# Performance work log

Hardware: AMD Instinct MI355X
Metric: run time of the kernel (lower is better)

## Reference

```python
import jax, jax.numpy as jnp
import numpy as np

N_NODES = 50000
N_EDGES = 800000
IN_DIM = 64
EDGE_DIM = 2
HID = 128
NUM_LAYERS = 4
NUM_GRAPHS = 128
BN_EPS = 1e-5


def setup_inputs() -> dict:
    key = jax.random.key(0)
    ks = jax.random.split(key, 24)
    s = 0.05
    inp = {
        "x": jax.random.normal(ks[0], (N_NODES, IN_DIM), jnp.float32),
        "edge_attr": jax.random.normal(ks[1], (N_EDGES, EDGE_DIM), jnp.float32),
        "edge_index": jax.random.randint(ks[2], (2, N_EDGES), 0, N_NODES, jnp.int32),
        "batch": jnp.sort(jax.random.randint(ks[3], (N_NODES,), 0, NUM_GRAPHS, jnp.int32)),
        # parameters
        "W_in": jax.random.normal(ks[4], (IN_DIM, HID), jnp.float32) * s,
        "b_in": jnp.zeros((HID,), jnp.float32),
        "W_e": jax.random.normal(ks[5], (EDGE_DIM, HID), jnp.float32) * s,
        "b_e": jnp.zeros((HID,), jnp.float32),
        "conv_W1": jax.random.normal(ks[6], (NUM_LAYERS, HID, HID), jnp.float32) * s,
        "conv_b1": jnp.zeros((NUM_LAYERS, HID), jnp.float32),
        "conv_W2": jax.random.normal(ks[7], (NUM_LAYERS, HID, HID), jnp.float32) * s,
        "conv_b2": jnp.zeros((NUM_LAYERS, HID), jnp.float32),
        "bn_g": jnp.ones((NUM_LAYERS, HID), jnp.float32),
        "bn_b": jnp.zeros((NUM_LAYERS, HID), jnp.float32),
        "vn_W1": jax.random.normal(ks[8], (HID, HID), jnp.float32) * s,
        "vn_b1": jnp.zeros((HID,), jnp.float32),
        "vn_W2": jax.random.normal(ks[9], (HID, HID), jnp.float32) * s,
        "vn_b2": jnp.zeros((HID,), jnp.float32),
        "cls_W1": jax.random.normal(ks[10], (HID, HID), jnp.float32) * s,
        "cls_b1": jnp.zeros((HID,), jnp.float32),
        "cls_W2": jax.random.normal(ks[11], (HID, 1), jnp.float32) * s,
        "cls_b2": jnp.zeros((1,), jnp.float32),
    }
    return inp


def reference(x, edge_attr, W_in, b_in, W_e, b_e, conv_W1, conv_b1, conv_W2, conv_b2,
              bn_g, bn_b, vn_W1, vn_b1, vn_W2, vn_b2, cls_W1, cls_b1, cls_W2, cls_b2,
              edge_index, batch):
    seg = jax.ops.segment_sum
    n = x.shape[0]
    src, dst = edge_index[0], edge_index[1]

    h = x @ W_in + b_in                      # [N, H]
    e = edge_attr @ W_e + b_e                # [E, H]
    vn = jnp.zeros((NUM_GRAPHS, HID), h.dtype)

    for i in range(NUM_LAYERS):
        h = h + vn[batch]                    # virtual-node broadcast
        # GINEConv (eps=0): msg = relu(x_j + e); aggregate-sum at dst; mlp(x_i + aggr)
        m = jax.nn.relu(h[src] + e)          # [E, H]
        aggr = seg(m, dst, num_segments=n)   # [N, H]
        z = h + aggr
        z = jax.nn.relu(z @ conv_W1[i] + conv_b1[i]) @ conv_W2[i] + conv_b2[i]
        # BatchNorm1d over node dim (batch statistics, biased variance)
        mu = jnp.mean(z, axis=0)
        var = jnp.mean(jnp.square(z - mu), axis=0)
        z = (z - mu) * jax.lax.rsqrt(var + BN_EPS) * bn_g[i] + bn_b[i]
        h = jax.nn.relu(z)                   # dropout disabled (deterministic)
        if i != NUM_LAYERS - 1:
            vn_up = seg(h, batch, num_segments=NUM_GRAPHS)   # global_add_pool
            vn = vn + (jax.nn.relu(vn_up @ vn_W1 + vn_b1) @ vn_W2 + vn_b2)

    # global_mean_pool
    counts = seg(jnp.ones((n,), h.dtype), batch, num_segments=NUM_GRAPHS)
    g = seg(h, batch, num_segments=NUM_GRAPHS) / jnp.maximum(counts, 1.0)[:, None]
    logits = (jax.nn.relu(g @ cls_W1 + cls_b1) @ cls_W2 + cls_b2).reshape(-1)
    return logits
```

## Files before the change

kernel.cpp:

```cpp
#include <hip/hip_runtime.h>

#define N_NODES 50000
#define N_EDGES 800000
#define IN_DIM 64
#define HID 128
#define NUM_LAYERS 4
#define NUM_GRAPHS 128
#define BN_EPS 1e-5f

typedef __attribute__((ext_vector_type(8))) short short8;
typedef __attribute__((ext_vector_type(4))) float f32x4;

__device__ inline unsigned short f2bf(float f) {
    unsigned int u = __float_as_uint(f);
    u += 0x7FFFu + ((u >> 16) & 1u);
    return (unsigned short)(u >> 16);
}
__device__ inline float bflo(unsigned int p) { return __uint_as_float(p << 16); }
__device__ inline float bfhi(unsigned int p) { return __uint_as_float(p & 0xFFFF0000u); }
__device__ inline float bfch(const uint4& v, int c) {
    unsigned int p = (&v.x)[c >> 1];
    return (c & 1) ? bfhi(p) : bflo(p);
}


__global__ void hist_kernel(const int* __restrict__ dst, int* __restrict__ cnt,
                            int* __restrict__ rank) {
    int base = blockIdx.x * 1024 + threadIdx.x;
#pragma unroll
    for (int u = 0; u < 4; ++u) {
        int e = base + u * 256;
        if (e < N_EDGES) rank[e] = atomicAdd(&cnt[dst[e]], 1);
    }
}

__global__ void endpos_kernel(const int* __restrict__ batch, int* __restrict__ endpos) {
    int n = blockIdx.x * 256 + threadIdx.x;
    if (n >= N_NODES) return;
    int b = batch[n];
    int b1 = (n + 1 < N_NODES) ? batch[n + 1] : NUM_GRAPHS;
    for (int g = b; g < b1; ++g) endpos[g] = n + 1;
    if (n == 0)
        for (int g = 0; g < b; ++g) endpos[g] = 0;
}

__global__ void wprep_kernel(const float* __restrict__ W_in,
                             const float* __restrict__ conv_W1,
                             const float* __restrict__ conv_W2,
                             unsigned short* __restrict__ wt_in,
                             unsigned short* __restrict__ wt1,
                             unsigned short* __restrict__ wt2) {
    int i = blockIdx.x * 256 + threadIdx.x;
    if (i < 128 * IN_DIM) {
        int c = i >> 6, k = i & 63;
        wt_in[i] = f2bf(W_in[k * HID + c]);
    }
    if (i < 4 * HID * HID) {
        int o = i & (HID * HID - 1);
        int layer = i >> 14;
        int c = o >> 7, k = o & 127;
        wt1[i] = f2bf(conv_W1[layer * HID * HID + k * HID + c]);
        wt2[i] = f2bf(conv_W2[layer * HID * HID + k * HID + c]);
    }
}

#define SCAN_BLOCKS ((N_NODES + 1023) / 1024)

__global__ __launch_bounds__(1024) void scan1_kernel(const int* __restrict__ cnt,
                                                     int* __restrict__ bsum) {
    __shared__ int ls[1024];
    int t = threadIdx.x;
    int g = blockIdx.x * 1024 + t;
    int v = (g < N_NODES) ? cnt[g] : 0;
    ls[t] = v;
    __syncthreads();
    for (int off = 512; off > 0; off >>= 1) {
        if (t < off) ls[t] += ls[t + off];
        __syncthreads();
    }
    if (t == 0) bsum[blockIdx.x] = ls[0];
}

__global__ void scan2_kernel(const int* __restrict__ bsum, int* __restrict__ boff) {
    if (threadIdx.x == 0) {
        int r = 0;
        for (int i = 0; i < SCAN_BLOCKS; ++i) {
            boff[i] = r;
            r += bsum[i];
        }
    }
}

__global__ __launch_bounds__(1024) void scan3_kernel(const int* __restrict__ cnt,
                                                     const int* __restrict__ boff,
                                                     int* __restrict__ row_start) {
    __shared__ int ls[1024];
    int t = threadIdx.x;
    int g = blockIdx.x * 1024 + t;
    int v = (g < N_NODES) ? cnt[g] : 0;
    ls[t] = v;
    __syncthreads();
    for (int off = 1; off < 1024; off <<= 1) {
        int x = (t >= off) ? ls[t - off] : 0;
        __syncthreads();
        ls[t] += x;
        __syncthreads();
    }
    int excl = ls[t] - v + boff[blockIdx.x];
    if (g < N_NODES) {
        row_start[g] = excl;
        if (g == N_NODES - 1) row_start[N_NODES] = excl + v;
    }
}

__global__ void fill_kernel(const int* __restrict__ src, const int* __restrict__ dst,
                            const float* __restrict__ ea, const int* __restrict__ rank,
                            const int* __restrict__ row_start, int4* __restrict__ edges) {
    int e = blockIdx.x * 256 + threadIdx.x;
    if (e >= N_EDGES) return;
    float2 a = *(const float2*)&ea[2 * e];
    int p = row_start[dst[e]] + rank[e];
    edges[p] = make_int4(src[e], __float_as_int(a.x), __float_as_int(a.y), 0);
}

__global__ void hvadd_kernel(const unsigned short* __restrict__ hbf,
                             const unsigned short* __restrict__ vnb,
                             const int* __restrict__ batch,
                             unsigned short* __restrict__ gbf) {
    int idx = blockIdx.x * 256 + threadIdx.x;
    int n = idx >> 4;
    if (n >= N_NODES) return;
    int cg = (idx & 15) * 8;
    uint4 h = *(const uint4*)&hbf[(size_t)n * HID + cg];
    uint4 v = *(const uint4*)&vnb[(size_t)batch[n] * HID + cg];
    unsigned int o[4];
#pragma unroll
    for (int p = 0; p < 4; ++p) {
        float lo = bflo((&h.x)[p]) + bflo((&v.x)[p]);
        float hi = bfhi((&h.x)[p]) + bfhi((&v.x)[p]);
        o[p] = (unsigned int)f2bf(lo) | ((unsigned int)f2bf(hi) << 16);
    }
    *(uint4*)&gbf[(size_t)n * HID + cg] = make_uint4(o[0], o[1], o[2], o[3]);
}

__global__ __launch_bounds__(256) void aggr_kernel(const unsigned short* __restrict__ gbf,
                                                   const int4* __restrict__ edges,
                                                   const int* __restrict__ row_start,
                                                   const float* __restrict__ We,
                                                   const float* __restrict__ be,
                                                   unsigned short* __restrict__ zbf,
                                                   float* __restrict__ S1,
                                                   float* __restrict__ S2) {
    int tid = threadIdx.x;
    if (blockIdx.x == 0 && tid < HID) {
        S1[tid] = 0.f;
        S2[tid] = 0.f;
    }
    int cg = (tid & 15) * 8;
    int n = blockIdx.x * 16 + (tid >> 4);

    float w0[8], w1[8], bc[8];
    {
        float4 a0 = *(const float4*)&We[cg], a1 = *(const float4*)&We[cg + 4];
        float4 b0 = *(const float4*)&We[HID + cg], b1v = *(const float4*)&We[HID + cg + 4];
        float4 c0 = *(const float4*)&be[cg], c1 = *(const float4*)&be[cg + 4];
        w0[0]=a0.x; w0[1]=a0.y; w0[2]=a0.z; w0[3]=a0.w; w0[4]=a1.x; w0[5]=a1.y; w0[6]=a1.z; w0[7]=a1.w;
        w1[0]=b0.x; w1[1]=b0.y; w1[2]=b0.z; w1[3]=b0.w; w1[4]=b1v.x; w1[5]=b1v.y; w1[6]=b1v.z; w1[7]=b1v.w;
        bc[0]=c0.x; bc[1]=c0.y; bc[2]=c0.z; bc[3]=c0.w; bc[4]=c1.x; bc[5]=c1.y; bc[6]=c1.z; bc[7]=c1.w;
    }

    uint4 hs = *(const uint4*)&gbf[(size_t)n * HID + cg];
    int jb = row_start[n], je = row_start[n + 1];
    float acc[8];
#pragma unroll
    for (int c = 0; c < 8; ++c) acc[c] = 0.f;

    int j = jb;
    for (; j + 8 <= je; j += 8) {
        int4 q[8];
        uint4 hq[8];
#pragma unroll
        for (int u = 0; u < 8; ++u) q[u] = edges[j + u];
#pragma unroll
        for (int u = 0; u < 8; ++u) hq[u] = *(const uint4*)&gbf[(size_t)q[u].x * HID + cg];
#pragma unroll
        for (int u = 0; u < 8; ++u) {
            float ex = __int_as_float(q[u].y), ey = __int_as_float(q[u].z);
#pragma unroll
            for (int c = 0; c < 8; ++c)
                acc[c] += fmaxf(bfch(hq[u], c) + fmaf(ex, w0[c], fmaf(ey, w1[c], bc[c])), 0.f);
        }
    }
    if (j + 4 <= je) {
        int4 q[4];
        uint4 hq[4];
#pragma unroll
        for (int u = 0; u < 4; ++u) q[u] = edges[j + u];
#pragma unroll
        for (int u = 0; u < 4; ++u) hq[u] = *(const uint4*)&gbf[(size_t)q[u].x * HID + cg];
#pragma unroll
        for (int u = 0; u < 4; ++u) {
            float ex = __int_as_float(q[u].y), ey = __int_as_float(q[u].z);
#pragma unroll
            for (int c = 0; c < 8; ++c)
                acc[c] += fmaxf(bfch(hq[u], c) + fmaf(ex, w0[c], fmaf(ey, w1[c], bc[c])), 0.f);
        }
        j += 4;
    }
    for (; j < je; ++j) {
        int4 q = edges[j];
        uint4 hq = *(const uint4*)&gbf[(size_t)q.x * HID + cg];
        float ex = __int_as_float(q.y), ey = __int_as_float(q.z);
#pragma unroll
        for (int c = 0; c < 8; ++c)
            acc[c] += fmaxf(bfch(hq, c) + fmaf(ex, w0[c], fmaf(ey, w1[c], bc[c])), 0.f);
    }

    unsigned int o[4];
#pragma unroll
    for (int p = 0; p < 4; ++p)
        o[p] = (unsigned int)f2bf(bflo((&hs.x)[p]) + acc[2 * p]) |
               ((unsigned int)f2bf(bfhi((&hs.x)[p]) + acc[2 * p + 1]) << 16);
    *(uint4*)&zbf[(size_t)n * HID + cg] = make_uint4(o[0], o[1], o[2], o[3]);
}

__global__ __launch_bounds__(256) void ingemm_kernel(const float* __restrict__ A,
                                                     const unsigned short* __restrict__ Wt,
                                                     const float* __restrict__ bias,
                                                     unsigned short* __restrict__ outbf) {
    constexpr int KD = IN_DIM;
    __shared__ unsigned short aS[64 * KD];
    __shared__ unsigned short wS[128 * KD];
    int tid = threadIdx.x;
    int row0 = blockIdx.x * 64;

#pragma unroll
    for (int it = 0; it < (64 * KD) / (256 * 4); ++it) {
        int idx = it * 1024 + tid * 4;
        int r = idx / KD, k = idx % KD;
        int grow = row0 + r;
        float4 v = (grow < N_NODES) ? *(const float4*)&A[(size_t)grow * KD + k]
                                    : make_float4(0.f, 0.f, 0.f, 0.f);
        unsigned int d0 = (unsigned int)f2bf(v.x) | ((unsigned int)f2bf(v.y) << 16);
        unsigned int d1 = (unsigned int)f2bf(v.z) | ((unsigned int)f2bf(v.w) << 16);
        unsigned int byte = (unsigned int)(idx * 2) ^ (unsigned int)((r & 7) << 4);
        *(uint2*)((char*)aS + byte) = make_uint2(d0, d1);
    }
#pragma unroll
    for (int it = 0; it < (128 * KD) / (256 * 8); ++it) {
        int idx = it * 2048 + tid * 8;
        int c = idx / KD;
        uint4 v = *(const uint4*)&Wt[idx];
        unsigned int byte = (unsigned int)(idx * 2) ^ (unsigned int)((c & 7) << 4);
        *(uint4*)((char*)wS + byte) = v;
    }
    __syncthreads();

    int w = tid >> 6, l = tid & 63;
    int wr = w >> 1, wc = w & 1, lr = l & 15, kq = (l >> 4) * 8;
    f32x4 acc[2][4];
#pragma unroll
    for (int r = 0; r < 2; ++r)
#pragma unroll
        for (int t = 0; t < 4; ++t) acc[r][t] = (f32x4){0.f, 0.f, 0.f, 0.f};

#pragma unroll
    for (int sstep = 0; sstep < KD / 32; ++sstep) {
        int k0 = sstep * 32 + kq;
        int ar0 = 32 * wr + lr, ar1 = ar0 + 16;
        short8 af0 = *(short8*)((char*)aS + ((unsigned int)((ar0 * KD + k0) * 2) ^
                                            (unsigned int)((ar0 & 7) << 4)));
        short8 af1 = *(short8*)((char*)aS + ((unsigned int)((ar1 * KD + k0) * 2) ^
                                            (unsigned int)((ar1 & 7) << 4)));
#pragma unroll
        for (int t = 0; t < 4; ++t) {
            int col = 64 * wc + 16 * t + lr;
            short8 bf = *(short8*)((char*)wS + ((unsigned int)((col * KD + k0) * 2) ^
                                               (unsigned int)((col & 7) << 4)));
            acc[0][t] = __builtin_amdgcn_mfma_f32_16x16x32_bf16(af0, bf, acc[0][t], 0, 0, 0);
            acc[1][t] = __builtin_amdgcn_mfma_f32_16x16x32_bf16(af1, bf, acc[1][t], 0, 0, 0);
        }
    }
#pragma unroll
    for (int r = 0; r < 2; ++r) {
        int rbase = row0 + 32 * wr + 16 * r + (l >> 4) * 4;
#pragma unroll
        for (int t = 0; t < 4; ++t) {
            int col = 64 * wc + 16 * t + lr;
            float b = bias[col];
#pragma unroll
            for (int q = 0; q < 4; ++q) {
                int grow = rbase + q;
                if (grow < N_NODES) outbf[(size_t)grow * HID + col] = f2bf(acc[r][t][q] + b);
            }
        }
    }
}

__global__ __launch_bounds__(512) void conv_kernel(const unsigned short* __restrict__ zbf,
                                                   const unsigned short* __restrict__ Wt1,
                                                   const float* __restrict__ b1,
                                                   const unsigned short* __restrict__ Wt2,
                                                   const float* __restrict__ b2,
                                                   float* __restrict__ B,
                                                   float* __restrict__ S1,
                                                   float* __restrict__ S2,
                                                   float* __restrict__ zinit, int zinit_n) {
    constexpr int KD = HID;
    __shared__ unsigned short aS[128 * KD];
    __shared__ unsigned short wS[128 * KD];
    __shared__ float sh1[HID], sh2[HID];
    int tid = threadIdx.x;
    if (zinit && blockIdx.x == 0)
        for (int i = tid; i < zinit_n; i += 512) zinit[i] = 0.f;
    if (tid < HID) { sh1[tid] = 0.f; sh2[tid] = 0.f; }

    int row0 = blockIdx.x * 128;

#pragma unroll
    for (int it = 0; it < 4; ++it) {
        int idx = it * 4096 + tid * 8;
        int r = idx >> 7;
        int grow = row0 + r;
        uint4 v = (grow < N_NODES) ? *(const uint4*)&zbf[(size_t)grow * HID + (idx & 127)]
                                   : make_uint4(0u, 0u, 0u, 0u);
        unsigned int byte = (unsigned int)(idx * 2) ^ (unsigned int)((r & 7) << 4);
        *(uint4*)((char*)aS + byte) = v;
    }
#pragma unroll
    for (int it = 0; it < 4; ++it) {
        int idx = it * 4096 + tid * 8;
        int c = idx >> 7;
        uint4 v = *(const uint4*)&Wt1[idx];
        unsigned int byte = (unsigned int)(idx * 2) ^ (unsigned int)((c & 7) << 4);
        *(uint4*)((char*)wS + byte) = v;
    }
    __syncthreads();

    int w = tid >> 6, l = tid & 63;
    int wr = w >> 2, wc = w & 3;
    int lr = l & 15, kq = (l >> 4) * 8;

    f32x4 acc[4][2];
#pragma unroll
    for (int rt = 0; rt < 4; ++rt)
#pragma unroll
        for (int ct = 0; ct < 2; ++ct) acc[rt][ct] = (f32x4){0.f, 0.f, 0.f, 0.f};

#pragma unroll
    for (int sstep = 0; sstep < 4; ++sstep) {
        int k0 = sstep * 32 + kq;
        short8 af[4];
#pragma unroll
        for (int rt = 0; rt < 4; ++rt) {
            int ar = 64 * wr + 16 * rt + lr;
            af[rt] = *(short8*)((char*)aS + ((unsigned int)((ar * KD + k0) * 2) ^
                                            (unsigned int)((ar & 7) << 4)));
        }
#pragma unroll
        for (int ct = 0; ct < 2; ++ct) {
            int col = 32 * wc + 16 * ct + lr;
            short8 bf = *(short8*)((char*)wS + ((unsigned int)((col * KD + k0) * 2) ^
                                               (unsigned int)((col & 7) << 4)));
#pragma unroll
            for (int rt = 0; rt < 4; ++rt)
                acc[rt][ct] = __builtin_amdgcn_mfma_f32_16x16x32_bf16(af[rt], bf, acc[rt][ct], 0, 0, 0);
        }
    }
    __syncthreads();

#pragma unroll
    for (int rt = 0; rt < 4; ++rt) {
        int lrow0 = 64 * wr + 16 * rt + (l >> 4) * 4;
#pragma unroll
        for (int ct = 0; ct < 2; ++ct) {
            int col = 32 * wc + 16 * ct + lr;
            float b = b1[col];
#pragma unroll
            for (int q = 0; q < 4; ++q) {
                int lrow = lrow0 + q;
                float v = fmaxf(acc[rt][ct][q] + b, 0.f);
                unsigned int byte = (unsigned int)((lrow * KD + col) * 2) ^
                                    (unsigned int)((lrow & 7) << 4);
                *(unsigned short*)((char*)aS + byte) = f2bf(v);
            }
        }
    }
#pragma unroll
    for (int it = 0; it < 4; ++it) {
        int idx = it * 4096 + tid * 8;
        int c = idx >> 7;
        uint4 v = *(const uint4*)&Wt2[idx];
        unsigned int byte = (unsigned int)(idx * 2) ^ (unsigned int)((c & 7) << 4);
        *(uint4*)((char*)wS + byte) = v;
    }
    __syncthreads();

    f32x4 acc2[4][2];
#pragma unroll
    for (int rt = 0; rt < 4; ++rt)
#pragma unroll
        for (int ct = 0; ct < 2; ++ct) acc2[rt][ct] = (f32x4){0.f, 0.f, 0.f, 0.f};

#pragma unroll
    for (int sstep = 0; sstep < 4; ++sstep) {
        int k0 = sstep * 32 + kq;
        short8 af[4];
#pragma unroll
        for (int rt = 0; rt < 4; ++rt) {
            int ar = 64 * wr + 16 * rt + lr;
            af[rt] = *(short8*)((char*)aS + ((unsigned int)((ar * KD + k0) * 2) ^
                                            (unsigned int)((ar & 7) << 4)));
        }
#pragma unroll
        for (int ct = 0; ct < 2; ++ct) {
            int col = 32 * wc + 16 * ct + lr;
            short8 bf = *(short8*)((char*)wS + ((unsigned int)((col * KD + k0) * 2) ^
                                               (unsigned int)((col & 7) << 4)));
#pragma unroll
            for (int rt = 0; rt < 4; ++rt)
                acc2[rt][ct] = __builtin_amdgcn_mfma_f32_16x16x32_bf16(af[rt], bf, acc2[rt][ct], 0, 0, 0);
        }
    }

#pragma unroll
    for (int rt = 0; rt < 4; ++rt) {
        int rbase = row0 + 64 * wr + 16 * rt + (l >> 4) * 4;
#pragma unroll
        for (int ct = 0; ct < 2; ++ct) {
            int col = 32 * wc + 16 * ct + lr;
            float b = b2[col];
            float s1 = 0.f, s2 = 0.f;
#pragma unroll
            for (int q = 0; q < 4; ++q) {
                int grow = rbase + q;
                if (grow < N_NODES) {
                    float v = acc2[rt][ct][q] + b;
                    B[(size_t)grow * HID + col] = v;
                    s1 += v;
                    s2 += v * v;
                }
            }
            atomicAdd(&sh1[col], s1);
            atomicAdd(&sh2[col], s2);
        }
    }
    __syncthreads();
    if (tid < HID) {
        atomicAdd(&S1[tid], sh1[tid]);
        atomicAdd(&S2[tid], sh2[tid]);
    }
}

__global__ __launch_bounds__(256) void bn_kernel(const float* __restrict__ z2,
                                                 const float* __restrict__ S1,
                                                 const float* __restrict__ S2,
                                                 const float* __restrict__ gma,
                                                 const float* __restrict__ bta,
                                                 const int* __restrict__ batch,
                                                 unsigned short* __restrict__ hbf,
                                                 float* __restrict__ up) {
    int tid = threadIdx.x;
    int cg = (tid & 31) * 4;
    int n0 = (blockIdx.x * 8 + (tid >> 5)) * 16;
    const float inv = 1.f / (float)N_NODES;
    float4 s1 = *(const float4*)&S1[cg];
    float4 s2 = *(const float4*)&S2[cg];
    float4 g4 = *(const float4*)&gma[cg];
    float4 b4 = *(const float4*)&bta[cg];
    float mux = s1.x * inv, muy = s1.y * inv, muz = s1.z * inv, muw = s1.w * inv;
    float gmx = g4.x * rsqrtf(s2.x * inv - mux * mux + BN_EPS);
    float gmy = g4.y * rsqrtf(s2.y * inv - muy * muy + BN_EPS);
    float gmz = g4.z * rsqrtf(s2.z * inv - muz * muz + BN_EPS);
    float gmw = g4.w * rsqrtf(s2.w * inv - muw * muw + BN_EPS);

    float4 acc = make_float4(0.f, 0.f, 0.f, 0.f);
    int gcur = -1;
    for (int i = 0; i < 16; ++i) {
        int n = n0 + i;
        if (n >= N_NODES) break;
        float4 v = *(const float4*)&z2[(size_t)n * HID + cg];
        float4 hn;
        hn.x = fmaxf(fmaf(v.x - mux, gmx, b4.x), 0.f);
        hn.y = fmaxf(fmaf(v.y - muy, gmy, b4.y), 0.f);
        hn.z = fmaxf(fmaf(v.z - muz, gmz, b4.z), 0.f);
        hn.w = fmaxf(fmaf(v.w - muw, gmw, b4.w), 0.f);
        uint2 pk;
        pk.x = (unsigned int)f2bf(hn.x) | ((unsigned int)f2bf(hn.y) << 16);
        pk.y = (unsigned int)f2bf(hn.z) | ((unsigned int)f2bf(hn.w) << 16);
        *(uint2*)&hbf[(size_t)n * HID + cg] = pk;
        int gb = batch[n];
        if (gb != gcur) {
            if (gcur >= 0) {
                atomicAdd(&up[gcur * HID + cg + 0], acc.x);
                atomicAdd(&up[gcur * HID + cg + 1], acc.y);
                atomicAdd(&up[gcur * HID + cg + 2], acc.z);
                atomicAdd(&up[gcur * HID + cg + 3], acc.w);
            }
            acc = make_float4(0.f, 0.f, 0.f, 0.f);
            gcur = gb;
        }
        acc.x += hn.x; acc.y += hn.y; acc.z += hn.z; acc.w += hn.w;
    }
    if (gcur >= 0) {
        atomicAdd(&up[gcur * HID + cg + 0], acc.x);
        atomicAdd(&up[gcur * HID + cg + 1], acc.y);
        atomicAdd(&up[gcur * HID + cg + 2], acc.z);
        atomicAdd(&up[gcur * HID + cg + 3], acc.w);
    }
}

__global__ __launch_bounds__(128) void vnmlp_kernel(const float* __restrict__ up,
                                                    const float* __restrict__ W1,
                                                    const float* __restrict__ b1,
                                                    const float* __restrict__ W2,
                                                    const float* __restrict__ b2,
                                                    float* __restrict__ vn,
                                                    unsigned short* __restrict__ vnb) {
    __shared__ float t[HID];
    int g = blockIdx.x, c = threadIdx.x;
    float s = b1[c];
#pragma unroll 8
    for (int k = 0; k < HID; ++k) s = fmaf(up[g * HID + k], W1[k * HID + c], s);
    t[c] = fmaxf(s, 0.f);
    __syncthreads();
    float s2 = b2[c];
#pragma unroll 8
    for (int k = 0; k < HID; ++k) s2 = fmaf(t[k], W2[k * HID + c], s2);
    float nv = vn[g * HID + c] + s2;
    vn[g * HID + c] = nv;
    vnb[g * HID + c] = f2bf(nv);
}

__global__ __launch_bounds__(128) void cls_kernel(const float* __restrict__ pool,
                                                  const int* __restrict__ endpos,
                                                  const float* __restrict__ W1,
                                                  const float* __restrict__ b1,
                                                  const float* __restrict__ W2,
                                                  const float* __restrict__ b2,
                                                  float* __restrict__ out) {
    __shared__ float t[HID];
    __shared__ float red[HID];
    int g = blockIdx.x, c = threadIdx.x;
    int cnt = endpos[g] - (g > 0 ? endpos[g - 1] : 0);
    float cntf = fmaxf((float)cnt, 1.f);
    t[c] = pool[g * HID + c] / cntf;
    __syncthreads();
    float s = b1[c];
#pragma unroll 8
    for (int k = 0; k < HID; ++k) s = fmaf(t[k], W1[k * HID + c], s);
    float y = fmaxf(s, 0.f);
    red[c] = y * W2[c];
    __syncthreads();
    for (int off = 64; off > 0; off >>= 1) {
        if (c < off) red[c] += red[c + off];
        __syncthreads();
    }
    if (c == 0) out[g] = red[0] + b2[0];
}

extern "C" void kernel_launch(void* const* d_in, const int* in_sizes, int n_in,
                              void* d_out, int out_size, void* d_ws, size_t ws_size,
                              hipStream_t stream) {
    const float* x        = (const float*)d_in[0];
    const float* edge_attr= (const float*)d_in[1];
    const int*   edge_idx = (const int*)d_in[2];
    const int*   batch    = (const int*)d_in[3];
    const float* W_in     = (const float*)d_in[4];
    const float* b_in     = (const float*)d_in[5];
    const float* W_e      = (const float*)d_in[6];
    const float* b_e      = (const float*)d_in[7];
    const float* conv_W1  = (const float*)d_in[8];
    const float* conv_b1  = (const float*)d_in[9];
    const float* conv_W2  = (const float*)d_in[10];
    const float* conv_b2  = (const float*)d_in[11];
    const float* bn_g     = (const float*)d_in[12];
    const float* bn_b     = (const float*)d_in[13];
    const float* vn_W1    = (const float*)d_in[14];
    const float* vn_b1    = (const float*)d_in[15];
    const float* vn_W2    = (const float*)d_in[16];
    const float* vn_b2    = (const float*)d_in[17];
    const float* cls_W1   = (const float*)d_in[18];
    const float* cls_b1   = (const float*)d_in[19];
    const float* cls_W2   = (const float*)d_in[20];
    const float* cls_b2   = (const float*)d_in[21];

    char* ws = (char*)d_ws;
    size_t off = 0;
    auto alloc = [&](size_t bytes) -> void* {
        void* p = ws + off;
        off = (off + bytes + 255) & ~(size_t)255;
        return p;
    };
    float* B = (float*)alloc((size_t)N_NODES * HID * 4);
    unsigned short* hbf = (unsigned short*)alloc((size_t)N_NODES * HID * 2);
    unsigned short* gbf = (unsigned short*)alloc((size_t)N_NODES * HID * 2);
    unsigned short* zbf = (unsigned short*)alloc((size_t)N_NODES * HID * 2);
    size_t zero_begin = off;
    int*   cnt    = (int*)alloc((size_t)N_NODES * 4);
    float* vn     = (float*)alloc((size_t)NUM_GRAPHS * HID * 4);
    unsigned short* vnb = (unsigned short*)alloc((size_t)NUM_GRAPHS * HID * 2);
    float* pool   = (float*)alloc((size_t)NUM_GRAPHS * HID * 4);
    size_t zero_end = off;
    int*    endpos    = (int*)alloc((size_t)NUM_GRAPHS * 4);
    int*    row_start = (int*)alloc((size_t)(N_NODES + 1) * 4);
    int*    rank      = (int*)alloc((size_t)N_EDGES * 4);
    int4*   edges     = (int4*)alloc((size_t)N_EDGES * 16);
    float*  vn_up     = (float*)alloc((size_t)NUM_GRAPHS * HID * 4);
    float*  S1        = (float*)alloc((size_t)HID * 4);
    float*  S2        = (float*)alloc((size_t)HID * 4);
    int*    bsum      = (int*)alloc((size_t)SCAN_BLOCKS * 4);
    int*    boff      = (int*)alloc((size_t)SCAN_BLOCKS * 4);
    unsigned short* wt_in = (unsigned short*)alloc((size_t)HID * IN_DIM * 2);
    unsigned short* wt1   = (unsigned short*)alloc((size_t)NUM_LAYERS * HID * HID * 2);
    unsigned short* wt2   = (unsigned short*)alloc((size_t)NUM_LAYERS * HID * HID * 2);
    (void)ws_size; (void)in_sizes; (void)n_in; (void)out_size;

    const int* srcp = edge_idx;
    const int* dstp = edge_idx + N_EDGES;

    hipMemsetAsync(ws + zero_begin, 0, zero_end - zero_begin, stream);
    hist_kernel<<<(N_EDGES + 1023) / 1024, 256, 0, stream>>>(dstp, cnt, rank);
    endpos_kernel<<<(N_NODES + 255) / 256, 256, 0, stream>>>(batch, endpos);
    wprep_kernel<<<(4 * HID * HID + 255) / 256, 256, 0, stream>>>(W_in, conv_W1, conv_W2,
                                                                  wt_in, wt1, wt2);
    scan1_kernel<<<SCAN_BLOCKS, 1024, 0, stream>>>(cnt, bsum);
    scan2_kernel<<<1, 64, 0, stream>>>(bsum, boff);
    scan3_kernel<<<SCAN_BLOCKS, 1024, 0, stream>>>(cnt, boff, row_start);
    fill_kernel<<<(N_EDGES + 255) / 256, 256, 0, stream>>>(srcp, dstp, edge_attr, rank,
                                                           row_start, edges);

    ingemm_kernel<<<(N_NODES + 63) / 64, 256, 0, stream>>>(x, wt_in, b_in, hbf);

    const int conv_grid = (N_NODES + 127) / 128;
    for (int i = 0; i < NUM_LAYERS; ++i) {
        const unsigned short* src_tab = hbf;
        if (i > 0) {
            hvadd_kernel<<<(N_NODES * 16 + 255) / 256, 256, 0, stream>>>(hbf, vnb, batch, gbf);
            src_tab = gbf;
        }
        aggr_kernel<<<N_NODES / 16, 256, 0, stream>>>(src_tab, edges, row_start,
                                                      W_e, b_e, zbf, S1, S2);
        conv_kernel<<<conv_grid, 512, 0, stream>>>(
            zbf, wt1 + (size_t)i * HID * HID, conv_b1 + (size_t)i * HID,
            wt2 + (size_t)i * HID * HID, conv_b2 + (size_t)i * HID,
            B, S1, S2, (i < NUM_LAYERS - 1) ? vn_up : nullptr, NUM_GRAPHS * HID);
        bn_kernel<<<(N_NODES + 127) / 128, 256, 0, stream>>>(B, S1, S2, bn_g + (size_t)i * HID,
                                                             bn_b + (size_t)i * HID, batch, hbf,
                                                             (i < NUM_LAYERS - 1) ? vn_up : pool);
        if (i < NUM_LAYERS - 1)
            vnmlp_kernel<<<NUM_GRAPHS, 128, 0, stream>>>(vn_up, vn_W1, vn_b1, vn_W2, vn_b2,
                                                         vn, vnb);
    }

    cls_kernel<<<NUM_GRAPHS, 128, 0, stream>>>(pool, endpos, cls_W1, cls_b1, cls_W2, cls_b2,
                                               (float*)d_out);
}
```

Baseline: 492.5 us.

## Store conv output as bf16 and reduce BN stats with wave shuffles

The second conv GEMM output is now written as bf16 instead of fp32, and bn_kernel reads bf16, halving the intermediate's write and read traffic. BN statistics are still computed from the fp32 values before rounding. Per-thread partial sums are accumulated across row tiles and reduced with xor shuffles before fewer LDS atomics are issued. Rounding z2 to bf16 before normalization adds some numerical error.

```diff
diff --git a/kernel.cpp b/kernel.cpp
--- a/kernel.cpp
+++ b/kernel.cpp
@@ -302,7 +302,7 @@
                                                    const float* __restrict__ b1,
                                                    const unsigned short* __restrict__ Wt2,
                                                    const float* __restrict__ b2,
-                                                   float* __restrict__ B,
+                                                   unsigned short* __restrict__ z2bf,
                                                    float* __restrict__ S1,
                                                    float* __restrict__ S2,
                                                    float* __restrict__ zinit, int zinit_n) {
@@ -423,6 +423,7 @@
         }
     }
 
+    float s1v[2] = {0.f, 0.f}, s2v[2] = {0.f, 0.f};
 #pragma unroll
     for (int rt = 0; rt < 4; ++rt) {
         int rbase = row0 + 64 * wr + 16 * rt + (l >> 4) * 4;
@@ -430,19 +431,27 @@
         for (int ct = 0; ct < 2; ++ct) {
             int col = 32 * wc + 16 * ct + lr;
             float b = b2[col];
-            float s1 = 0.f, s2 = 0.f;
 #pragma unroll
             for (int q = 0; q < 4; ++q) {
                 int grow = rbase + q;
                 if (grow < N_NODES) {
                     float v = acc2[rt][ct][q] + b;
-                    B[(size_t)grow * HID + col] = v;
-                    s1 += v;
-                    s2 += v * v;
+                    z2bf[(size_t)grow * HID + col] = f2bf(v);
+                    s1v[ct] += v;
+                    s2v[ct] += v * v;
                 }
             }
-            atomicAdd(&sh1[col], s1);
-            atomicAdd(&sh2[col], s2);
+        }
+    }
+#pragma unroll
+    for (int ct = 0; ct < 2; ++ct) {
+        float a = s1v[ct], bsum2 = s2v[ct];
+        a += __shfl_xor(a, 16); a += __shfl_xor(a, 32);
+        bsum2 += __shfl_xor(bsum2, 16); bsum2 += __shfl_xor(bsum2, 32);
+        if ((l >> 4) == 0) {
+            int col = 32 * wc + 16 * ct + lr;
+            atomicAdd(&sh1[col], a);
+            atomicAdd(&sh2[col], bsum2);
         }
     }
     __syncthreads();
@@ -452,7 +461,7 @@
     }
 }
 
-__global__ __launch_bounds__(256) void bn_kernel(const float* __restrict__ z2,
+__global__ __launch_bounds__(256) void bn_kernel(const unsigned short* __restrict__ z2bf,
                                                  const float* __restrict__ S1,
                                                  const float* __restrict__ S2,
                                                  const float* __restrict__ gma,
@@ -479,12 +488,12 @@
     for (int i = 0; i < 16; ++i) {
         int n = n0 + i;
         if (n >= N_NODES) break;
-        float4 v = *(const float4*)&z2[(size_t)n * HID + cg];
+        uint2 zv = *(const uint2*)&z2bf[(size_t)n * HID + cg];
         float4 hn;
-        hn.x = fmaxf(fmaf(v.x - mux, gmx, b4.x), 0.f);
-        hn.y = fmaxf(fmaf(v.y - muy, gmy, b4.y), 0.f);
-        hn.z = fmaxf(fmaf(v.z - muz, gmz, b4.z), 0.f);
-        hn.w = fmaxf(fmaf(v.w - muw, gmw, b4.w), 0.f);
+        hn.x = fmaxf(fmaf(bflo(zv.x) - mux, gmx, b4.x), 0.f);
+        hn.y = fmaxf(fmaf(bfhi(zv.x) - muy, gmy, b4.y), 0.f);
+        hn.z = fmaxf(fmaf(bflo(zv.y) - muz, gmz, b4.z), 0.f);
+        hn.w = fmaxf(fmaf(bfhi(zv.y) - muw, gmw, b4.w), 0.f);
         uint2 pk;
         pk.x = (unsigned int)f2bf(hn.x) | ((unsigned int)f2bf(hn.y) << 16);
         pk.y = (unsigned int)f2bf(hn.z) | ((unsigned int)f2bf(hn.w) << 16);
@@ -592,7 +601,7 @@
         off = (off + bytes + 255) & ~(size_t)255;
         return p;
     };
-    float* B = (float*)alloc((size_t)N_NODES * HID * 4);
+    unsigned short* z2bf = (unsigned short*)alloc((size_t)N_NODES * HID * 2);
     unsigned short* hbf = (unsigned short*)alloc((size_t)N_NODES * HID * 2);
     unsigned short* gbf = (unsigned short*)alloc((size_t)N_NODES * HID * 2);
     unsigned short* zbf = (unsigned short*)alloc((size_t)N_NODES * HID * 2);
@@ -644,8 +653,8 @@
         conv_kernel<<<conv_grid, 512, 0, stream>>>(
             zbf, wt1 + (size_t)i * HID * HID, conv_b1 + (size_t)i * HID,
             wt2 + (size_t)i * HID * HID, conv_b2 + (size_t)i * HID,
-            B, S1, S2, (i < NUM_LAYERS - 1) ? vn_up : nullptr, NUM_GRAPHS * HID);
-        bn_kernel<<<(N_NODES + 127) / 128, 256, 0, stream>>>(B, S1, S2, bn_g + (size_t)i * HID,
+            z2bf, S1, S2, (i < NUM_LAYERS - 1) ? vn_up : nullptr, NUM_GRAPHS * HID);
+        bn_kernel<<<(N_NODES + 127) / 128, 256, 0, stream>>>(z2bf, S1, S2, bn_g + (size_t)i * HID,
                                                              bn_b + (size_t)i * HID, batch, hbf,
                                                              (i < NUM_LAYERS - 1) ? vn_up : pool);
         if (i < NUM_LAYERS - 1)
```

Result: faster. 431.5 us (-12.4%).
